# Kernel tuning notes

Hardware: AMD Instinct MI355X
Metric: run time of the kernel (lower is better)

Reference implementation:

```python
import jax, jax.numpy as jnp
import numpy as np

NUM_CLASSES = 7
B = 14336
D = 512
H_KDE = 0.2          # sklearn KernelDensity(bandwidth=0.2, kernel='gaussian')
KERNEL_MUL = 2.0
KERNEL_NUM = 5
BN_EPS = 1e-5


def _pairwise_sqdist(a, b):
    # ||a_i - b_j||^2 via gram trick; avoids the [n,n,d] broadcast tensor the torch code builds
    an = jnp.sum(a * a, axis=-1)
    bn = jnp.sum(b * b, axis=-1)
    d2 = an[:, None] + bn[None, :] - 2.0 * (a @ b.T)
    return jnp.maximum(d2, 0.0)


def _multi_kernel(total):
    # sum of KERNEL_NUM Gaussian kernels, bandwidths 1.25 * 2^i (bandwidth=5 / 2^(5//2))
    d2 = _pairwise_sqdist(total, total)
    bw0 = 5.0 / (KERNEL_MUL ** (KERNEL_NUM // 2))
    k = jnp.zeros_like(d2)
    for i in range(KERNEL_NUM):  # small fixed loop, avoids [5,n,n] intermediate
        k = k + jnp.exp(-d2 / (bw0 * (KERNEL_MUL ** i)))
    return k


def _mmd(src, tgt):
    m = src.shape[0]
    k = _multi_kernel(jnp.concatenate([src, tgt], axis=0))
    return jnp.mean(k[:m, :m] + k[m:, m:] - k[:m, m:] - k[m:, :m])


def _kde_weight(class_feats):
    # sklearn gaussian KDE: log p(x_i) = logsumexp_j(-||x_i-x_j||^2 / (2 h^2)) - log m - (d/2) log(2 pi h^2)
    # volume v = sum_i 1 / log p(x_i); weight = 1 / (v + 1e-5)
    C, m, d = class_feats.shape
    log_norm = -0.5 * d * jnp.log(2.0 * jnp.pi * (H_KDE ** 2)) - jnp.log(jnp.float32(m))

    def one(f):
        d2 = _pairwise_sqdist(f, f)
        logp = jax.nn.logsumexp(-d2 / (2.0 * (H_KDE ** 2)), axis=1) + log_norm
        return jnp.sum(1.0 / logp)

    v = jax.vmap(one)(class_feats)
    return 1.0 / (v + 1e-5)


def setup_inputs() -> dict:
    key = jax.random.key(0)
    k1, k2 = jax.random.split(key)
    fea = jax.random.normal(k1, (B, D), dtype=jnp.float32) * 0.05
    W_fc = jax.random.normal(k2, (NUM_CLASSES, D), dtype=jnp.float32) * 0.02
    gamma = jnp.ones((NUM_CLASSES,), dtype=jnp.float32)
    beta = jnp.zeros((NUM_CLASSES,), dtype=jnp.float32)
    # balanced, contiguous class blocks so per-class splits are static reshapes
    targets = jnp.repeat(jnp.arange(NUM_CLASSES, dtype=jnp.int32), B // NUM_CLASSES)
    return {"fea": fea, "W_fc": W_fc, "gamma": gamma, "beta": beta, "targets": targets}


def reference(fea, W_fc, gamma, beta, targets):
    Bn, d = fea.shape
    C = NUM_CLASSES
    m = Bn // C

    # out = BatchNorm1d(fc(fea)) in train mode (biased batch stats)
    logits = fea @ W_fc.T                              # [B, C]
    mu = jnp.mean(logits, axis=0)
    var = jnp.var(logits, axis=0)
    out = gamma * (logits - mu) / jnp.sqrt(var + BN_EPS) + beta

    # split_feature_makeLD with balanced contiguous targets -> static reshape
    cf = fea.reshape(C, m, d)                          # [C, m, D]

    # KDE density weights: computed on detached numpy features in the original -> stop_gradient
    w = jax.lax.stop_gradient(_kde_weight(cf))         # [C]

    def per_class(i):
        src = cf[i]
        # remove_element concatenates classes 0..i-1, i+1..C-1 in order;
        # first m rows of that = class 0 (class 1 when i == 0)
        tgt = cf[jnp.where(i > 0, 0, 1)]
        return _mmd(src, tgt)

    losses = jax.vmap(per_class)(jnp.arange(C))        # [C]
    affinity_loss = -jnp.sum(losses * w)
    return (out, affinity_loss)
```

## Files before the change

### kernel.cpp

```cpp
#include <hip/hip_runtime.h>

#define B_ROWS 14336
#define D_DIM  512
#define C_CLS  7
#define M_CLS  2048

typedef __attribute__((ext_vector_type(4))) float f32x4;

#define FP8_SCALE 64.0f
#define INV_2S2   (2.0f / 4096.0f)

typedef const __attribute__((address_space(1))) char gchar_t;
typedef __attribute__((address_space(3))) char lchar_t;

__device__ __forceinline__ void gload16(const char* g, char* l) {
  __builtin_amdgcn_global_load_lds((gchar_t*)g, (lchar_t*)l, 16, 0, 0);
}

__global__ __launch_bounds__(256) void k_prep(const float* __restrict__ fea,
                                              const float* __restrict__ W,
                                              char* __restrict__ f8p,
                                              float* __restrict__ an,
                                              float* __restrict__ logits,
                                              float* __restrict__ zb) {
  int t = threadIdx.x, wave = t >> 6, lane = t & 63;
  if (blockIdx.x == 0 && t < 64) zb[t] = 0.f;
  __shared__ char lrow[16 * 528];

  int r0 = blockIdx.x * 16;
#pragma unroll
  for (int k = 0; k < 4; ++k) {
    int rl = wave * 4 + k;
    int row = r0 + rl;
    const float4* fr4 = (const float4*)(fea + (size_t)row * D_DIM);
    float4 v0 = fr4[lane * 2], v1 = fr4[lane * 2 + 1];

    float p[8];
#pragma unroll
    for (int c = 0; c < 7; ++c) {
      const float4* w4 = (const float4*)(W + c * D_DIM);
      float4 q0 = w4[lane * 2], q1 = w4[lane * 2 + 1];
      p[c] = v0.x * q0.x + v0.y * q0.y + v0.z * q0.z + v0.w * q0.w +
             v1.x * q1.x + v1.y * q1.y + v1.z * q1.z + v1.w * q1.w;
    }
    p[7] = v0.x * v0.x + v0.y * v0.y + v0.z * v0.z + v0.w * v0.w +
           v1.x * v1.x + v1.y * v1.y + v1.z * v1.z + v1.w * v1.w;

#pragma unroll
    for (int c = 0; c < 8; ++c) {
      p[c] += __shfl_xor(p[c], 1);
      p[c] += __shfl_xor(p[c], 2);
      p[c] += __shfl_xor(p[c], 4);
    }
    int v = lane & 7;
    float y = p[0];
    y = (v == 1) ? p[1] : y;
    y = (v == 2) ? p[2] : y;
    y = (v == 3) ? p[3] : y;
    y = (v == 4) ? p[4] : y;
    y = (v == 5) ? p[5] : y;
    y = (v == 6) ? p[6] : y;
    y = (v == 7) ? p[7] : y;
    y += __shfl_xor(y, 8);
    y += __shfl_xor(y, 16);
    y += __shfl_xor(y, 32);
    if (lane < 7) logits[row * 7 + lane] = y;
    else if (lane == 7) an[row] = y;

    int w0 = __builtin_amdgcn_cvt_pk_fp8_f32(v0.x * FP8_SCALE, v0.y * FP8_SCALE, 0, 0);
    w0     = __builtin_amdgcn_cvt_pk_fp8_f32(v0.z * FP8_SCALE, v0.w * FP8_SCALE, w0, 1);
    int w1 = __builtin_amdgcn_cvt_pk_fp8_f32(v1.x * FP8_SCALE, v1.y * FP8_SCALE, 0, 0);
    w1     = __builtin_amdgcn_cvt_pk_fp8_f32(v1.z * FP8_SCALE, v1.w * FP8_SCALE, w1, 1);
    *(int2*)&lrow[rl * 528 + lane * 8] = make_int2(w0, w1);
  }
  __syncthreads();
  int4* outp = (int4*)f8p + (size_t)blockIdx.x * 512;
#pragma unroll
  for (int pi = 0; pi < 2; ++pi) {
    int idx = pi * 256 + t;
    int kp = idx >> 6, l = idx & 63;
    int sr = l & 15, qk = l >> 4;
    int2 lo = *(const int2*)&lrow[sr * 528 + kp * 64 + qk * 8];
    int2 hi = *(const int2*)&lrow[sr * 528 + kp * 64 + 32 + qk * 8];
    outp[idx] = make_int4(lo.x, lo.y, hi.x, hi.y);
  }
}

__global__ __launch_bounds__(512, 2) void k_gram(const char* __restrict__ f8p,
                                                 const float* __restrict__ an,
                                                 const float* __restrict__ logits,
                                                 float* __restrict__ S,
                                                 float* __restrict__ rs_part,
                                                 float* __restrict__ S1,
                                                 float* __restrict__ S2,
                                                 float* __restrict__ aff) {
  int x = blockIdx.x & 7, u = blockIdx.x >> 3;
  int t = threadIdx.x, lane = t & 63, wave = t >> 6;
  if (blockIdx.x == 0 && t == 0) aff[0] = 0.f;

  if (u == 80) {
    if (x >= 7) return;
    int c = x, seg = wave;
    int r0 = seg * 1792;
    float s1 = 0.f, s2 = 0.f;
    for (int j = lane; j < 1792; j += 64) {
      float v = logits[(size_t)(r0 + j) * 7 + c];
      s1 += v;
      s2 += v * v;
    }
#pragma unroll
    for (int o = 1; o < 64; o <<= 1) {
      s1 += __shfl_xor(s1, o);
      s2 += __shfl_xor(s2, o);
    }
    if (lane == 0) { atomicAdd(&S1[c], s1); atomicAdd(&S2[c], s2); }
    return;
  }

  int cls1, cls2, ti, tj, Sidx;
  bool self;
  if (x < 7 && u < 36) {
    int a = 0, r = u;
    while (r > a) { r -= a + 1; ++a; }
    ti = a; tj = r;
    cls1 = x; cls2 = x; Sidx = x; self = true;
  } else {
    int j;
    if (x < 7) j = x * 44 + (u - 36);
    else { if (u >= 76) return; j = 308 + u; }
    int p = j >> 6, t64 = j & 63;
    ti = t64 >> 3; tj = t64 & 7;
    cls1 = p + 1; cls2 = 0; Sidx = 7 + p; self = false;
  }

  __shared__ char ldsA[2][16384];
  __shared__ char ldsB[16384];
  __shared__ float bacc[8];

  int R0 = cls1 * 2048 + ti * 256;
  int C0 = cls2 * 2048 + tj * 256;

  const char* gA0 = f8p + ((size_t)(R0 >> 4) + wave * 2)     * 8192 + lane * 16;
  const char* gA1 = f8p + ((size_t)(R0 >> 4) + wave * 2 + 1) * 8192 + lane * 16;
  const char* gB0 = f8p + ((size_t)(C0 >> 4) + wave * 2)     * 8192 + lane * 16;
  const char* gB1 = f8p + ((size_t)(C0 >> 4) + wave * 2 + 1) * 8192 + lane * 16;

  int wr = wave >> 2, wc = wave & 3;
  int q = lane >> 4, s = lane & 15;

  f32x4 acc[8][4];
#pragma unroll
  for (int i = 0; i < 8; ++i)
#pragma unroll
    for (int j = 0; j < 4; ++j)
      acc[i][j] = (f32x4){0.f, 0.f, 0.f, 0.f};

  gload16(gA0, &ldsA[0][(wave * 2) * 1024 + lane * 16]);
  gload16(gA1, &ldsA[0][(wave * 2 + 1) * 1024 + lane * 16]);
  gload16(gB0, &ldsB[(wave * 2) * 1024 + lane * 16]);
  gload16(gB1, &ldsB[(wave * 2 + 1) * 1024 + lane * 16]);
  __syncthreads();

#define MM16(A0_, A1_, I0_, I1_)                                              \
  do {                                                                        \
    asm volatile("s_waitcnt lgkmcnt(0)" ::: "memory");                        \
    __builtin_amdgcn_sched_barrier(0);                                        \
    __builtin_amdgcn_s_setprio(1);                                            \
    _Pragma("unroll")                                                         \
    for (int j_ = 0; j_ < 4; ++j_)                                            \
      acc[I0_][j_] = __builtin_amdgcn_mfma_f32_16x16x32_fp8_fp8(              \
          A0_.x, bb[j_].x, acc[I0_][j_], 0, 0, 0);                            \
    _Pragma("unroll")                                                         \
    for (int j_ = 0; j_ < 4; ++j_)                                            \
      acc[I1_][j_] = __builtin_amdgcn_mfma_f32_16x16x32_fp8_fp8(              \
          A1_.x, bb[j_].x, acc[I1_][j_], 0, 0, 0);                            \
    _Pragma("unroll")                                                         \
    for (int j_ = 0; j_ < 4; ++j_)                                            \
      acc[I0_][j_] = __builtin_amdgcn_mfma_f32_16x16x32_fp8_fp8(              \
          A0_.y, bb[j_].y, acc[I0_][j_], 0, 0, 0);                            \
    _Pragma("unroll")                                                         \
    for (int j_ = 0; j_ < 4; ++j_)                                            \
      acc[I1_][j_] = __builtin_amdgcn_mfma_f32_16x16x32_fp8_fp8(              \
          A1_.y, bb[j_].y, acc[I1_][j_], 0, 0, 0);                            \
    __builtin_amdgcn_s_setprio(0);                                            \
  } while (0)

#pragma unroll 1
  for (int kt = 0; kt < 8; ++kt) {
    int cur = kt & 1;
    const char* LA = &ldsA[cur][(wr * 8) * 1024 + lane * 16];
    const char* LB = &ldsB[(wc * 4) * 1024 + lane * 16];
    longlong2 a0, a1, bb[4];
    a0 = *(const longlong2*)(LA);
    a1 = *(const longlong2*)(LA + 1024);
#pragma unroll
    for (int j = 0; j < 4; ++j) bb[j] = *(const longlong2*)(LB + j * 1024);
    if (kt < 7) {
      int nb = cur ^ 1;
      gload16(gA0 + (kt + 1) * 1024, &ldsA[nb][(wave * 2) * 1024 + lane * 16]);
      gload16(gA1 + (kt + 1) * 1024, &ldsA[nb][(wave * 2 + 1) * 1024 + lane * 16]);
    }
    MM16(a0, a1, 0, 1);
    a0 = *(const longlong2*)(LA + 2 * 1024);
    a1 = *(const longlong2*)(LA + 3 * 1024);
    __builtin_amdgcn_s_barrier();
    asm volatile("" ::: "memory");
    if (kt < 7) {
      gload16(gB0 + (kt + 1) * 1024, &ldsB[(wave * 2) * 1024 + lane * 16]);
      gload16(gB1 + (kt + 1) * 1024, &ldsB[(wave * 2 + 1) * 1024 + lane * 16]);
    }
    MM16(a0, a1, 2, 3);
    a0 = *(const longlong2*)(LA + 4 * 1024);
    a1 = *(const longlong2*)(LA + 5 * 1024);
    __builtin_amdgcn_s_barrier();
    asm volatile("" ::: "memory");
    MM16(a0, a1, 4, 5);
    a0 = *(const longlong2*)(LA + 6 * 1024);
    a1 = *(const longlong2*)(LA + 7 * 1024);
    __builtin_amdgcn_s_barrier();
    asm volatile("" ::: "memory");
    MM16(a0, a1, 6, 7);
    if (kt < 7)
      asm volatile("s_waitcnt vmcnt(0)" ::: "memory");
    __builtin_amdgcn_s_barrier();
    asm volatile("" ::: "memory");
  }
#undef MM16

  bool dg = self && (ti == tj);
  bool mirror = self && (ti > tj);
  float blockAcc = 0.f;
  float colAcc[4] = {0.f, 0.f, 0.f, 0.f};
  float anB_[4];
#pragma unroll
  for (int j = 0; j < 4; ++j) anB_[j] = an[C0 + wc * 64 + j * 16 + s];

#pragma unroll
  for (int i = 0; i < 8; ++i) {
    f32x4 anA_ = *(const f32x4*)&an[R0 + wr * 128 + i * 16 + q * 4];
#pragma unroll
    for (int rg = 0; rg < 4; ++rg) {
      int rl = wr * 128 + i * 16 + q * 4 + rg;
      float aA = anA_[rg];
      float rowAcc = 0.f;
#pragma unroll
      for (int j = 0; j < 4; ++j) {
        int cl = wc * 64 + j * 16 + s;
        float g = acc[i][j][rg];
        float d2 = fmaxf(aA + anB_[j] - g * INV_2S2, 0.f);
        if (dg && rl == cl) d2 = 0.f;
        float e1 = __expf(-0.05f * d2);
        float e2 = e1 * e1, e4 = e2 * e2, e8 = e4 * e4, e16 = e8 * e8;
        blockAcc += e1 + e2 + e4 + e8 + e16;
        if (self) {
          float ek = __expf(-12.5f * d2);
          rowAcc += ek;
          if (mirror) colAcc[j] += ek;
        }
      }
      if (self) {
        rowAcc += __shfl_xor(rowAcc, 1);
        rowAcc += __shfl_xor(rowAcc, 2);
        rowAcc += __shfl_xor(rowAcc, 4);
        rowAcc += __shfl_xor(rowAcc, 8);
        if (s == 0)
          rs_part[(size_t)(R0 + rl) * 48 + tj * 4 + wc] = rowAcc;
      }
    }
  }
  if (mirror) {
#pragma unroll
    for (int j = 0; j < 4; ++j) {
      float v = colAcc[j];
      v += __shfl_xor(v, 16);
      v += __shfl_xor(v, 32);
      if (q == 0)
        rs_part[(size_t)(C0 + wc * 64 + j * 16 + s) * 48 + 32 + ti * 2 + wr] = v;
    }
    blockAcc *= 2.f;
  }
#pragma unroll
  for (int o = 1; o < 64; o <<= 1) blockAcc += __shfl_xor(blockAcc, o);
  if (lane == 0) bacc[wave] = blockAcc;
  __syncthreads();
  if (t == 0) {
    float sB = 0.f;
#pragma unroll
    for (int w = 0; w < 8; ++w) sB += bacc[w];
    atomicAdd(&S[Sidx], sB);
  }
}

__global__ __launch_bounds__(1024) void k_final(const float* __restrict__ logits,
                                                const float* __restrict__ S1,
                                                const float* __restrict__ S2,
                                                const float* __restrict__ gamma,
                                                const float* __restrict__ beta,
                                                const float* __restrict__ rs_part,
                                                const float* __restrict__ S,
                                                float* __restrict__ out) {
  int b = blockIdx.x, t = threadIdx.x;
  if (b < 98) {
    int idx = b * 1024 + t;
    int row = idx / 7;
    int c = idx - row * 7;
    float mu = S1[c] * (1.f / 14336.f);
    float var = S2[c] * (1.f / 14336.f) - mu * mu;
    out[idx] = gamma[c] * (logits[idx] - mu) * rsqrtf(var + 1e-5f) + beta[c];
    return;
  }
  int c = b - 98;
  const float LOG_NORM = 345.9110632f;
  float v = 0.f;
  for (int i = t; i < M_CLS; i += 1024) {
    int bi = i >> 8;
    const float* rp = rs_part + (size_t)(c * M_CLS + i) * 48;
    float rsum = 0.f;
    int nd = 4 * bi + 4;
    for (int k = 0; k < nd; ++k) rsum += rp[k];
    for (int k = 34 + 2 * bi; k < 48; ++k) rsum += rp[k];
    v += 1.f / (logf(rsum) + LOG_NORM);
  }
#pragma unroll
  for (int o = 1; o < 64; o <<= 1) v += __shfl_xor(v, o);
  __shared__ float r[16];
  if ((t & 63) == 0) r[t >> 6] = v;
  __syncthreads();
  if (t == 0) {
    float vs = 0.f;
#pragma unroll
    for (int w = 0; w < 16; ++w) vs += r[w];
    float w = 1.f / (vs + 1e-5f);
    const float inv_m2 = 1.0f / ((float)M_CLS * (float)M_CLS);
    float Ssrc = S[c];
    float Stgt = (c > 0) ? S[0] : S[1];
    float X    = (c > 0) ? S[6 + c] : S[7];
    float mmd = (Ssrc + Stgt - 2.f * X) * inv_m2;
    atomicAdd(&out[100352], -mmd * w);
  }
}

extern "C" void kernel_launch(void* const* d_in, const int* in_sizes, int n_in,
                              void* d_out, int out_size, void* d_ws, size_t ws_size,
                              hipStream_t stream) {
  const float* fea   = (const float*)d_in[0];
  const float* W_fc  = (const float*)d_in[1];
  const float* gamma = (const float*)d_in[2];
  const float* beta  = (const float*)d_in[3];
  float* out = (float*)d_out;

  char* ws = (char*)d_ws;
  char* f8p = ws;
  float* fbase   = (float*)(ws + 7340032);
  float* an      = fbase;
  float* logits  = fbase + 14336;
  float* zb      = fbase + 114688;
  float* S1      = zb;
  float* S2      = zb + 7;
  float* S       = zb + 16;
  float* rs_part = fbase + 114752;

  k_prep <<<896, 256, 0, stream>>>(fea, W_fc, f8p, an, logits, zb);
  k_gram <<<648, 512, 0, stream>>>(f8p, an, logits, S, rs_part, S1, S2,
                                   out + 100352);
  k_final<<<105, 1024, 0, stream>>>(logits, S1, S2, gamma, beta, rs_part, S, out);
}
```

Measured before the change: 186.4 us.

## Load B fragments directly from global into registers, dropping B LDS staging

The B operand tiles are now read by each wave straight from global memory into registers (double-buffered even/odd sets), no longer staged through a shared LDS buffer via global_load_lds. The k-loop is unrolled by two so register buffers alternate, with vmcnt waits adjusted to track the outstanding loads. This removes the B LDS traffic and the associated ds_reads, shrinking LDS use. In exchange, each wave issues redundant global loads for the same B data (four waves share a column group), register pressure rises, and the hand-tuned vmcnt counts must stay correct.

```diff
diff --git a/kernel.cpp b/kernel.cpp
--- a/kernel.cpp
+++ b/kernel.cpp
@@ -134,19 +134,17 @@
   }
 
   __shared__ char ldsA[2][16384];
-  __shared__ char ldsB[16384];
   __shared__ float bacc[8];
 
   int R0 = cls1 * 2048 + ti * 256;
   int C0 = cls2 * 2048 + tj * 256;
 
+  int wr = wave >> 2, wc = wave & 3;
+  int q = lane >> 4, s = lane & 15;
+
   const char* gA0 = f8p + ((size_t)(R0 >> 4) + wave * 2)     * 8192 + lane * 16;
   const char* gA1 = f8p + ((size_t)(R0 >> 4) + wave * 2 + 1) * 8192 + lane * 16;
-  const char* gB0 = f8p + ((size_t)(C0 >> 4) + wave * 2)     * 8192 + lane * 16;
-  const char* gB1 = f8p + ((size_t)(C0 >> 4) + wave * 2 + 1) * 8192 + lane * 16;
-
-  int wr = wave >> 2, wc = wave & 3;
-  int q = lane >> 4, s = lane & 15;
+  const char* gB  = f8p + ((size_t)(C0 >> 4) + wc * 4) * 8192 + lane * 16;
 
   f32x4 acc[8][4];
 #pragma unroll
@@ -155,13 +153,15 @@
     for (int j = 0; j < 4; ++j)
       acc[i][j] = (f32x4){0.f, 0.f, 0.f, 0.f};
 
+  longlong2 bbE[4], bbO[4];
+#pragma unroll
+  for (int j = 0; j < 4; ++j)
+    bbE[j] = *(const longlong2*)(gB + j * 8192);
   gload16(gA0, &ldsA[0][(wave * 2) * 1024 + lane * 16]);
   gload16(gA1, &ldsA[0][(wave * 2 + 1) * 1024 + lane * 16]);
-  gload16(gB0, &ldsB[(wave * 2) * 1024 + lane * 16]);
-  gload16(gB1, &ldsB[(wave * 2 + 1) * 1024 + lane * 16]);
   __syncthreads();
 
-#define MM16(A0_, A1_, I0_, I1_)                                              \
+#define MM16(BB_, A0_, A1_, I0_, I1_)                                         \
   do {                                                                        \
     asm volatile("s_waitcnt lgkmcnt(0)" ::: "memory");                        \
     __builtin_amdgcn_sched_barrier(0);                                        \
@@ -169,61 +169,90 @@
     _Pragma("unroll")                                                         \
     for (int j_ = 0; j_ < 4; ++j_)                                            \
       acc[I0_][j_] = __builtin_amdgcn_mfma_f32_16x16x32_fp8_fp8(              \
-          A0_.x, bb[j_].x, acc[I0_][j_], 0, 0, 0);                            \
+          A0_.x, BB_[j_].x, acc[I0_][j_], 0, 0, 0);                           \
     _Pragma("unroll")                                                         \
     for (int j_ = 0; j_ < 4; ++j_)                                            \
       acc[I1_][j_] = __builtin_amdgcn_mfma_f32_16x16x32_fp8_fp8(              \
-          A1_.x, bb[j_].x, acc[I1_][j_], 0, 0, 0);                            \
+          A1_.x, BB_[j_].x, acc[I1_][j_], 0, 0, 0);                           \
     _Pragma("unroll")                                                         \
     for (int j_ = 0; j_ < 4; ++j_)                                            \
       acc[I0_][j_] = __builtin_amdgcn_mfma_f32_16x16x32_fp8_fp8(              \
-          A0_.y, bb[j_].y, acc[I0_][j_], 0, 0, 0);                            \
+          A0_.y, BB_[j_].y, acc[I0_][j_], 0, 0, 0);                           \
     _Pragma("unroll")                                                         \
     for (int j_ = 0; j_ < 4; ++j_)                                            \
       acc[I1_][j_] = __builtin_amdgcn_mfma_f32_16x16x32_fp8_fp8(              \
-          A1_.y, bb[j_].y, acc[I1_][j_], 0, 0, 0);                            \
+          A1_.y, BB_[j_].y, acc[I1_][j_], 0, 0, 0);                           \
     __builtin_amdgcn_s_setprio(0);                                            \
   } while (0)
 
 #pragma unroll 1
-  for (int kt = 0; kt < 8; ++kt) {
-    int cur = kt & 1;
-    const char* LA = &ldsA[cur][(wr * 8) * 1024 + lane * 16];
-    const char* LB = &ldsB[(wc * 4) * 1024 + lane * 16];
-    longlong2 a0, a1, bb[4];
-    a0 = *(const longlong2*)(LA);
-    a1 = *(const longlong2*)(LA + 1024);
-#pragma unroll
-    for (int j = 0; j < 4; ++j) bb[j] = *(const longlong2*)(LB + j * 1024);
-    if (kt < 7) {
-      int nb = cur ^ 1;
-      gload16(gA0 + (kt + 1) * 1024, &ldsA[nb][(wave * 2) * 1024 + lane * 16]);
-      gload16(gA1 + (kt + 1) * 1024, &ldsA[nb][(wave * 2 + 1) * 1024 + lane * 16]);
-    }
-    MM16(a0, a1, 0, 1);
-    a0 = *(const longlong2*)(LA + 2 * 1024);
-    a1 = *(const longlong2*)(LA + 3 * 1024);
-    __builtin_amdgcn_s_barrier();
-    asm volatile("" ::: "memory");
-    if (kt < 7) {
-      gload16(gB0 + (kt + 1) * 1024, &ldsB[(wave * 2) * 1024 + lane * 16]);
-      gload16(gB1 + (kt + 1) * 1024, &ldsB[(wave * 2 + 1) * 1024 + lane * 16]);
-    }
-    MM16(a0, a1, 2, 3);
-    a0 = *(const longlong2*)(LA + 4 * 1024);
-    a1 = *(const longlong2*)(LA + 5 * 1024);
-    __builtin_amdgcn_s_barrier();
-    asm volatile("" ::: "memory");
-    MM16(a0, a1, 4, 5);
-    a0 = *(const longlong2*)(LA + 6 * 1024);
-    a1 = *(const longlong2*)(LA + 7 * 1024);
-    __builtin_amdgcn_s_barrier();
-    asm volatile("" ::: "memory");
-    MM16(a0, a1, 6, 7);
-    if (kt < 7)
-      asm volatile("s_waitcnt vmcnt(0)" ::: "memory");
-    __builtin_amdgcn_s_barrier();
-    asm volatile("" ::: "memory");
+  for (int h = 0; h < 4; ++h) {
+    {
+      const char* LA = &ldsA[0][(wr * 8) * 1024 + lane * 16];
+      longlong2 a0, a1;
+      a0 = *(const longlong2*)(LA);
+      a1 = *(const longlong2*)(LA + 1024);
+      gload16(gA0 + (2 * h + 1) * 1024, &ldsA[1][(wave * 2) * 1024 + lane * 16]);
+      gload16(gA1 + (2 * h + 1) * 1024, &ldsA[1][(wave * 2 + 1) * 1024 + lane * 16]);
+      MM16(bbE, a0, a1, 0, 1);
+      a0 = *(const longlong2*)(LA + 2 * 1024);
+      a1 = *(const longlong2*)(LA + 3 * 1024);
+      __builtin_amdgcn_s_barrier();
+      asm volatile("" ::: "memory");
+#pragma unroll
+      for (int j = 0; j < 4; ++j)
+        bbO[j] = *(const longlong2*)(gB + j * 8192 + (2 * h + 1) * 1024);
+      MM16(bbE, a0, a1, 2, 3);
+      a0 = *(const longlong2*)(LA + 4 * 1024);
+      a1 = *(const longlong2*)(LA + 5 * 1024);
+      __builtin_amdgcn_s_barrier();
+      asm volatile("" ::: "memory");
+      MM16(bbE, a0, a1, 4, 5);
+      a0 = *(const longlong2*)(LA + 6 * 1024);
+      a1 = *(const longlong2*)(LA + 7 * 1024);
+      __builtin_amdgcn_s_barrier();
+      asm volatile("" ::: "memory");
+      MM16(bbE, a0, a1, 6, 7);
+      asm volatile("s_waitcnt vmcnt(4)" ::: "memory");
+      __builtin_amdgcn_s_barrier();
+      asm volatile("" ::: "memory");
+    }
+    {
+      const char* LA = &ldsA[1][(wr * 8) * 1024 + lane * 16];
+      longlong2 a0, a1;
+      a0 = *(const longlong2*)(LA);
+      a1 = *(const longlong2*)(LA + 1024);
+      if (h < 3) {
+        gload16(gA0 + (2 * h + 2) * 1024, &ldsA[0][(wave * 2) * 1024 + lane * 16]);
+        gload16(gA1 + (2 * h + 2) * 1024, &ldsA[0][(wave * 2 + 1) * 1024 + lane * 16]);
+      }
+      MM16(bbO, a0, a1, 0, 1);
+      a0 = *(const longlong2*)(LA + 2 * 1024);
+      a1 = *(const longlong2*)(LA + 3 * 1024);
+      __builtin_amdgcn_s_barrier();
+      asm volatile("" ::: "memory");
+      if (h < 3) {
+#pragma unroll
+        for (int j = 0; j < 4; ++j)
+          bbE[j] = *(const longlong2*)(gB + j * 8192 + (2 * h + 2) * 1024);
+      }
+      MM16(bbO, a0, a1, 2, 3);
+      a0 = *(const longlong2*)(LA + 4 * 1024);
+      a1 = *(const longlong2*)(LA + 5 * 1024);
+      __builtin_amdgcn_s_barrier();
+      asm volatile("" ::: "memory");
+      MM16(bbO, a0, a1, 4, 5);
+      a0 = *(const longlong2*)(LA + 6 * 1024);
+      a1 = *(const longlong2*)(LA + 7 * 1024);
+      __builtin_amdgcn_s_barrier();
+      asm volatile("" ::: "memory");
+      MM16(bbO, a0, a1, 6, 7);
+      if (h < 3) {
+        asm volatile("s_waitcnt vmcnt(4)" ::: "memory");
+        __builtin_amdgcn_s_barrier();
+        asm volatile("" ::: "memory");
+      }
+    }
   }
 #undef MM16
 
```

Measured after the change: 192.8 us. 3.4% more time.
